# Optimization experiments

Measured on AMD Instinct MI355X. Metric: run time of the kernel, lower is better.

The kernel has to match this reference:

```python
import jax, jax.numpy as jnp
import numpy as np

IN_FEAT = 78
C = 128          # out_channels
H = 8            # nheads (layer 1)
B = 1024         # num graphs / batch
NPG = 32         # nodes per graph
N = B * NPG      # total nodes
EPG = 128        # edges per graph
E = B * EPG
GENE = 18000
PROT = 6688
FP = 2048        # drr/drc fingerprint size
N_TASKS = 1


def _lin(key, fan_in, fan_out):
    kw, kb = jax.random.split(key)
    s = 1.0 / np.sqrt(fan_in)
    W = jax.random.uniform(kw, (fan_in, fan_out), jnp.float32, -s, s)
    b = jax.random.uniform(kb, (fan_out,), jnp.float32, -s, s)
    return W, b


def setup_inputs() -> dict:
    key = jax.random.key(0)
    ks = jax.random.split(key, 32)
    goff = jnp.repeat(jnp.arange(B, dtype=jnp.int64) * NPG, EPG)
    e1s = jax.random.randint(ks[0], (E,), 0, NPG, dtype=jnp.int64) + goff
    e1d = jax.random.randint(ks[1], (E,), 0, NPG, dtype=jnp.int64) + goff
    e2s = jax.random.randint(ks[2], (E,), 0, NPG, dtype=jnp.int64) + goff
    e2d = jax.random.randint(ks[3], (E,), 0, NPG, dtype=jnp.int64) + goff
    inp = {
        "x1": jax.random.normal(ks[4], (N, IN_FEAT), jnp.float32),
        "x2": jax.random.normal(ks[5], (N, IN_FEAT), jnp.float32),
        "gene_exp": jax.random.uniform(ks[6], (B, GENE), jnp.float32),
        "drr": jax.random.uniform(ks[7], (B, FP), jnp.float32),
        "drc": jax.random.uniform(ks[8], (B, FP), jnp.float32),
        "prot_exp": jax.random.normal(ks[9], (B, PROT), jnp.float32),
        "edge_index1": jnp.stack([e1s, e1d]),
        "edge_index2": jnp.stack([e2s, e2d]),
        "batch": jnp.repeat(jnp.arange(B, dtype=jnp.int64), NPG),
    }
    W1, b1 = _lin(ks[10], IN_FEAT, H * C)
    inp.update(W_gat1=W1, b_gat1=b1,
               a_src1=jax.random.normal(ks[11], (H, C), jnp.float32) * 0.1,
               a_dst1=jax.random.normal(ks[12], (H, C), jnp.float32) * 0.1)
    # GAT layer 2: 1024 -> 128, 1 head
    W2, b2 = _lin(ks[13], H * C, C)
    inp.update(W_gat2=W2, b_gat2=b2,
               a_src2=jax.random.normal(ks[14], (1, C), jnp.float32) * 0.1,
               a_dst2=jax.random.normal(ks[15], (1, C), jnp.float32) * 0.1)
    inp["W_fcg"], inp["b_fcg"] = _lin(ks[16], C, C)
    # reduction MLP: gene -> 2048 -> 512 -> 2C
    inp["Wr1"], inp["br1"] = _lin(ks[17], GENE, 2048)
    inp["Wr2"], inp["br2"] = _lin(ks[18], 2048, 512)
    inp["Wr3"], inp["br3"] = _lin(ks[19], 512, 2 * C)
    # prot MLP: 6688 -> 1024 -> 512 -> 2C
    inp["Wp1"], inp["bp1"] = _lin(ks[20], PROT, 1024)
    inp["Wp2"], inp["bp2"] = _lin(ks[21], 1024, 512)
    inp["Wp3"], inp["bp3"] = _lin(ks[22], 512, 2 * C)
    # fingerprint fusion linears
    inp["Wdrr"], inp["bdrr"] = _lin(ks[23], C + FP, C + FP)
    inp["Wdrc"], inp["bdrc"] = _lin(ks[24], C + FP, C + FP)
    # predictor (3 layers): in = 2*(C+FP) + 2C + 2C = 4864 -> 512 -> 256 -> n_tasks
    in_dim = 2 * (C + FP) + 2 * C + 2 * C
    inp["Wf1"], inp["bf1"] = _lin(ks[25], in_dim, 512)
    inp["Wf2"], inp["bf2"] = _lin(ks[26], 512, 256)
    inp["Wout"], inp["bout"] = _lin(ks[27], 256, N_TASKS)
    return inp


def _gat(x, src, dst, W, a_src, a_dst, b, heads, ch):
    n = x.shape[0]
    # add self-loops (PyG GATConv default)
    sl = jnp.arange(n, dtype=src.dtype)
    src = jnp.concatenate([src, sl])
    dst = jnp.concatenate([dst, sl])
    h = (x @ W).reshape(n, heads, ch)                    # [N,H,C]
    a_s = (h * a_src).sum(-1)                            # [N,H]
    a_d = (h * a_dst).sum(-1)
    e = jax.nn.leaky_relu(a_s[src] + a_d[dst], 0.2)      # [E',H]
    m = jax.ops.segment_max(e, dst, num_segments=n)
    ex = jnp.exp(e - m[dst])
    den = jax.ops.segment_sum(ex, dst, num_segments=n)
    alpha = ex / (den[dst] + 1e-16)
    out = jax.ops.segment_sum(h[src] * alpha[:, :, None], dst, num_segments=n)
    return out.reshape(n, heads * ch) + b


def reference(x1, x2, gene_exp, drr, drc, prot_exp,
              W_gat1, b_gat1, a_src1, a_dst1,
              W_gat2, b_gat2, a_src2, a_dst2,
              W_fcg, b_fcg,
              Wr1, br1, Wr2, br2, Wr3, br3,
              Wp1, bp1, Wp2, bp2, Wp3, bp3,
              Wdrr, bdrr, Wdrc, bdrc,
              Wf1, bf1, Wf2, bf2, Wout, bout,
              edge_index1, edge_index2, batch):
    nb = gene_exp.shape[0]

    def drug_branch(x, ei):
        x = jax.nn.elu(_gat(x, ei[0], ei[1], W_gat1, a_src1, a_dst1, b_gat1, H, C))
        x = jax.nn.elu(_gat(x, ei[0], ei[1], W_gat2, a_src2, a_dst2, b_gat2, 1, C))
        x = jax.ops.segment_max(x, batch, num_segments=nb)   # global max pool
        return jax.nn.relu(x @ W_fcg + b_fcg)

    g1 = drug_branch(x1, edge_index1)
    g2 = drug_branch(x2, edge_index2)

    # gene branch: L2 row-normalize then MLP (dropout off at inference)
    norm = jnp.sqrt((gene_exp * gene_exp).sum(1, keepdims=True))
    cell = gene_exp / jnp.maximum(norm, 1e-12)
    cell = jax.nn.relu(cell @ Wr1 + br1)
    cell = jax.nn.relu(cell @ Wr2 + br2)
    cell_vec = jax.nn.relu(cell @ Wr3 + br3)

    # protein branch
    p = prot_exp.reshape(-1, PROT)
    p = jax.nn.elu(p @ Wp1 + bp1)
    p = jax.nn.elu(p @ Wp2 + bp2)
    p = jax.nn.relu(p @ Wp3 + bp3)

    # fingerprint fusion
    d1 = jnp.concatenate([g1, drr], axis=1)
    d2 = jnp.concatenate([g2, drc], axis=1)
    d1 = jax.nn.relu(d1 @ Wdrr + bdrr)
    d2 = jax.nn.relu(d2 @ Wdrc + bdrc)

    y = jnp.concatenate([d1, d2, cell_vec, p], axis=1)
    # 3-layer predictor
    y = jax.nn.relu(y @ Wf1 + bf1)
    y = jax.nn.relu(y @ Wf2 + bf2)
    out = y @ Wout + bout
    return out
```

## Files before the change

kernel.cpp:

```cpp
#include <hip/hip_runtime.h>
#include <math.h>

#define BATCH   1024
#define NPG     32
#define NNODES  (BATCH * NPG)
#define EPG     128
#define INFEAT  78
#define CCH     128
#define NHEAD   8
#define GENE    18000
#define GENEP   18048
#define PROT    6688
#define PROTP   6784
#define FPD     2048

#define ACT_NONE 0
#define ACT_RELU 1
#define ACT_ELU  2

typedef unsigned short ushort_t;
typedef __bf16 bf16x8_t __attribute__((ext_vector_type(8)));
typedef float  f32x4_t  __attribute__((ext_vector_type(4)));

__device__ __forceinline__ float b2f(ushort_t u) {
    return __uint_as_float(((unsigned)u) << 16);
}
__device__ __forceinline__ ushort_t f2b(float f) {
    unsigned x = __float_as_uint(f);
    return (ushort_t)((x + 0x7fffu + ((x >> 16) & 1u)) >> 16);
}

#define GBM 128
#define GBN 128
#define GBK 32

__device__ __forceinline__ void gemm_core(
    const ushort_t* __restrict__ A, const ushort_t* __restrict__ BT,
    int K, int kb, int ke, int row0, int col0,
    ushort_t* Asl, ushort_t* Bsl, f32x4_t acc[4][4])
{
    const int tid  = threadIdx.x;
    const int wave = tid >> 6;
    const int lane = tid & 63;
    const int wr   = wave >> 1;
    const int wc   = wave & 1;
    const int srow = lane >> 2;
    const int skel = (lane & 3) * 8;

    for (int k0 = kb; k0 < ke; k0 += GBK) {
        __syncthreads();
        #pragma unroll
        for (int t = 0; t < 2; ++t) {
            const int rg = wave * 32 + t * 16;
            const ushort_t* ga = A + (size_t)(row0 + rg + srow) * K + k0 + skel;
            __builtin_amdgcn_global_load_lds(
                (const __attribute__((address_space(1))) void*)ga,
                (__attribute__((address_space(3))) void*)&Asl[rg * GBK], 16, 0, 0);
            const ushort_t* gb = BT + (size_t)(col0 + rg + srow) * K + k0 + skel;
            __builtin_amdgcn_global_load_lds(
                (const __attribute__((address_space(1))) void*)gb,
                (__attribute__((address_space(3))) void*)&Bsl[rg * GBK], 16, 0, 0);
        }
        __syncthreads();

        const int fr = lane & 15;
        const int fq = lane >> 4;
        bf16x8_t av[4], bv[4];
        #pragma unroll
        for (int i = 0; i < 4; ++i)
            av[i] = *(const bf16x8_t*)&Asl[(wr * 64 + i * 16 + fr) * GBK + fq * 8];
        #pragma unroll
        for (int j = 0; j < 4; ++j)
            bv[j] = *(const bf16x8_t*)&Bsl[(wc * 64 + j * 16 + fr) * GBK + fq * 8];
        #pragma unroll
        for (int i = 0; i < 4; ++i)
            #pragma unroll
            for (int j = 0; j < 4; ++j)
                acc[i][j] = __builtin_amdgcn_mfma_f32_16x16x32_bf16(
                    av[i], bv[j], acc[i][j], 0, 0, 0);
    }
}

__global__ __launch_bounds__(256) void gemm_bf16_kernel(
    const ushort_t* __restrict__ A, const ushort_t* __restrict__ BT,
    const float* __restrict__ bias, ushort_t* __restrict__ C,
    int M, int N, int K, int act)
{
    __shared__ ushort_t Asl[GBM * GBK];
    __shared__ ushort_t Bsl[GBN * GBK];
    const int lane = threadIdx.x & 63;
    const int wave = threadIdx.x >> 6;
    const int wr = wave >> 1, wc = wave & 1;
    const int row0 = blockIdx.y * GBM;
    const int col0 = blockIdx.x * GBN;

    f32x4_t acc[4][4] = {};
    gemm_core(A, BT, K, 0, K, row0, col0, Asl, Bsl, acc);

    const int fr = lane & 15;
    const int fq = lane >> 4;
    #pragma unroll
    for (int i = 0; i < 4; ++i) {
        #pragma unroll
        for (int j = 0; j < 4; ++j) {
            const int gn = col0 + wc * 64 + j * 16 + fr;
            const float bb = bias ? bias[gn] : 0.0f;
            #pragma unroll
            for (int r = 0; r < 4; ++r) {
                const int gm = row0 + wr * 64 + i * 16 + fq * 4 + r;
                float v = acc[i][j][r] + bb;
                if (act == ACT_RELU)     v = fmaxf(v, 0.0f);
                else if (act == ACT_ELU) v = (v > 0.0f) ? v : (expf(v) - 1.0f);
                C[(size_t)gm * N + gn] = f2b(v);
            }
        }
    }
}

__global__ __launch_bounds__(256) void gemm_bf16_part_kernel(
    const ushort_t* __restrict__ A, const ushort_t* __restrict__ BT,
    float* __restrict__ part, int M, int N, int K, int KC)
{
    __shared__ ushort_t Asl[GBM * GBK];
    __shared__ ushort_t Bsl[GBN * GBK];
    const int lane = threadIdx.x & 63;
    const int wave = threadIdx.x >> 6;
    const int wr = wave >> 1, wc = wave & 1;
    const int row0 = blockIdx.y * GBM;
    const int col0 = blockIdx.x * GBN;
    const int z    = blockIdx.z;
    const int kb   = z * KC;
    const int ke   = min(K, kb + KC);

    f32x4_t acc[4][4] = {};
    gemm_core(A, BT, K, kb, ke, row0, col0, Asl, Bsl, acc);

    const int fr = lane & 15;
    const int fq = lane >> 4;
    float* po = part + (size_t)z * M * N;
    #pragma unroll
    for (int i = 0; i < 4; ++i)
        #pragma unroll
        for (int j = 0; j < 4; ++j) {
            const int gn = col0 + wc * 64 + j * 16 + fr;
            #pragma unroll
            for (int r = 0; r < 4; ++r) {
                const int gm = row0 + wr * 64 + i * 16 + fq * 4 + r;
                po[(size_t)gm * N + gn] = acc[i][j][r];
            }
        }
}

__global__ __launch_bounds__(256) void reduce_kernel(
    const float* __restrict__ part, const float* __restrict__ bias,
    ushort_t* __restrict__ C, int MN, int N, int S, int act)
{
    int i4 = (blockIdx.x * 256 + threadIdx.x) * 4;
    if (i4 >= MN) return;
    float4 s = *(const float4*)&part[i4];
    for (int z = 1; z < S; ++z) {
        float4 v = *(const float4*)&part[(size_t)z * MN + i4];
        s.x += v.x; s.y += v.y; s.z += v.z; s.w += v.w;
    }
    const int n = i4 % N;
    float o[4] = { s.x, s.y, s.z, s.w };
    if (bias) { o[0] += bias[n]; o[1] += bias[n+1]; o[2] += bias[n+2]; o[3] += bias[n+3]; }
    unsigned pk[2];
    ushort_t r[4];
    #pragma unroll
    for (int k = 0; k < 4; ++k) {
        float v = o[k];
        if (act == ACT_RELU)     v = fmaxf(v, 0.0f);
        else if (act == ACT_ELU) v = (v > 0.0f) ? v : (expf(v) - 1.0f);
        r[k] = f2b(v);
    }
    pk[0] = (unsigned)r[0] | ((unsigned)r[1] << 16);
    pk[1] = (unsigned)r[2] | ((unsigned)r[3] << 16);
    *(uint2*)&C[i4] = make_uint2(pk[0], pk[1]);
}

#define DSREAD(dst, addr) asm volatile("ds_read_b128 %0, %1" : "=v"(dst) : "v"(addr))

template <int MH>
__device__ __forceinline__ void read_A8(bf16x8_t (&av)[4][2], unsigned b0, unsigned b1)
{
    DSREAD(av[0][0], b0 + (MH * 4 + 0) * 2048);
    DSREAD(av[0][1], b1 + (MH * 4 + 0) * 2048);
    DSREAD(av[1][0], b0 + (MH * 4 + 1) * 2048);
    DSREAD(av[1][1], b1 + (MH * 4 + 1) * 2048);
    DSREAD(av[2][0], b0 + (MH * 4 + 2) * 2048);
    DSREAD(av[2][1], b1 + (MH * 4 + 2) * 2048);
    DSREAD(av[3][0], b0 + (MH * 4 + 3) * 2048);
    DSREAD(av[3][1], b1 + (MH * 4 + 3) * 2048);
}

template <int NH>
__device__ __forceinline__ void read_B8(bf16x8_t (&bvh)[2][2], unsigned b0, unsigned b1)
{
    DSREAD(bvh[0][0], b0 + (NH * 2 + 0) * 2048);
    DSREAD(bvh[0][1], b1 + (NH * 2 + 0) * 2048);
    DSREAD(bvh[1][0], b0 + (NH * 2 + 1) * 2048);
    DSREAD(bvh[1][1], b1 + (NH * 2 + 1) * 2048);
}

template <int MH, int NH>
__device__ __forceinline__ void mfma_quad(const bf16x8_t (&av)[4][2],
                                          const bf16x8_t (&bvh)[2][2],
                                          f32x4_t (&acc)[8][4])
{
    #pragma unroll
    for (int qq = 0; qq < 4; ++qq)
        #pragma unroll
        for (int pp = 0; pp < 2; ++pp)
            #pragma unroll
            for (int ss = 0; ss < 2; ++ss)
                acc[MH * 4 + qq][NH * 2 + pp] = __builtin_amdgcn_mfma_f32_16x16x32_bf16(
                    av[qq][ss], bvh[pp][ss], acc[MH * 4 + qq][NH * 2 + pp], 0, 0, 0);
}

__device__ __forceinline__ void stage_half8(
    const ushort_t* __restrict__ G, int rc0, int K, int kt,
    unsigned lo0, ushort_t* smemp, int tid)
{
    const int lane = tid & 63;
    const int ce = (((lane & 7) ^ ((lane >> 3) & 7)) << 3);
    #pragma unroll
    for (int j = 0; j < 2; ++j) {
        const int rr = j * 64 + (tid >> 3);
        const ushort_t* g = G + (size_t)(rc0 + rr) * K + kt + ce;
        const unsigned lo = lo0 + (unsigned)((j * 64 + ((tid >> 3) & ~7)) * 128);
        __builtin_amdgcn_global_load_lds(
            (const __attribute__((address_space(1))) void*)g,
            (__attribute__((address_space(3))) void*)((char*)smemp + lo),
            16, 0, 0);
    }
}

#define PH_TAIL(MH, NH, BVH, VM) \
    __builtin_amdgcn_s_barrier(); \
    asm volatile("s_waitcnt lgkmcnt(0)"); \
    __builtin_amdgcn_sched_barrier(0); \
    __builtin_amdgcn_s_setprio(1); \
    mfma_quad<MH, NH>(av, BVH, acc); \
    __builtin_amdgcn_s_setprio(0); \
    __builtin_amdgcn_sched_barrier(0); \
    if (VM) asm volatile("s_waitcnt vmcnt(4)"); \
    __builtin_amdgcn_s_barrier();

__global__ __launch_bounds__(512, 2) void gemm_bf16_8ph_kernel(
    const ushort_t* __restrict__ A, const ushort_t* __restrict__ BT,
    float* __restrict__ part, int M, int N, int K, int IPC)
{
    extern __shared__ ushort_t smem8[];
    const int tid  = threadIdx.x;
    const int lane = tid & 63;
    const int wid  = tid >> 6;
    const int wm = wid >> 2, wn = wid & 3;
    const int fr = lane & 15, fq = lane >> 4;

    const int gx = N >> 8, gy = M >> 8;
    const int nwg = (int)gridDim.x;
    const int q8 = nwg >> 3, r8 = nwg & 7;
    const int xcd = (int)blockIdx.x & 7, sub = (int)blockIdx.x >> 3;
    const int wg = (xcd < r8 ? xcd * (q8 + 1) : r8 * (q8 + 1) + (xcd - r8) * q8) + sub;
    const int bz  = wg / (gx * gy);
    const int rem = wg - bz * gx * gy;
    const int by  = rem / gx;
    const int bx  = rem - by * gx;
    const int row0 = by << 8, col0 = bx << 8;

    const int iters = K >> 7;
    const int k0    = bz * IPC * 128;
    const int nit   = min(IPC, iters - bz * IPC);

    const unsigned SB  = (unsigned)(size_t)(__attribute__((address_space(3))) void*)smem8;
    const unsigned xa  = (unsigned)((fr & 7) << 4);
    const unsigned cs0 = ((unsigned)(fq * 16)) ^ xa;
    const unsigned cs1 = ((unsigned)(64 + fq * 16)) ^ xa;
    const unsigned arow = SB + (unsigned)((wm * 128 + fr) * 128);
    const unsigned brow = SB + 32768u + (unsigned)((wn * 64 + fr) * 128);

    f32x4_t  acc[8][4] = {};
    bf16x8_t av[4][2];
    bf16x8_t bv[2][2][2];

    auto KT = [&](int tt) { int kt = k0 + tt * 64; return kt > K - 64 ? K - 64 : kt; };
    auto STA = [&](int tt, int h) {
        stage_half8(A, row0 + h * 128, K, KT(tt),
                    (unsigned)(((tt & 1) * 65536) + h * 16384), smem8, tid);
    };
    auto STB = [&](int tt, int h) {
        stage_half8(BT, col0 + h * 128, K, KT(tt),
                    (unsigned)(((tt & 1) * 65536) + 32768 + h * 16384), smem8, tid);
    };

    STB(0, 0); STB(0, 1); STA(0, 0); STA(0, 1); STB(1, 0); STB(1, 1);
    asm volatile("s_waitcnt vmcnt(4)");
    __builtin_amdgcn_s_barrier();

    for (int it = 0; it < nit; ++it) {
        const int t = it << 1;
        read_A8<0>(av, arow + cs0, arow + cs1);
        read_B8<0>(bv[0], brow + cs0, brow + cs1);
        STA(t + 1, 0);
        PH_TAIL(0, 0, bv[0], 0)

        read_B8<1>(bv[1], brow + cs0, brow + cs1);
        STA(t + 1, 1);
        PH_TAIL(0, 1, bv[1], 0)

        read_A8<1>(av, arow + cs0, arow + cs1);
        STB(t + 2, 0);
        PH_TAIL(1, 0, bv[0], 0)

        STB(t + 2, 1);
        PH_TAIL(1, 1, bv[1], 1)

        read_A8<0>(av, arow + 65536u + cs0, arow + 65536u + cs1);
        read_B8<0>(bv[0], brow + 65536u + cs0, brow + 65536u + cs1);
        STA(t + 2, 0);
        PH_TAIL(0, 0, bv[0], 0)

        read_B8<1>(bv[1], brow + 65536u + cs0, brow + 65536u + cs1);
        STA(t + 2, 1);
        PH_TAIL(0, 1, bv[1], 0)

        read_A8<1>(av, arow + 65536u + cs0, arow + 65536u + cs1);
        STB(t + 3, 0);
        PH_TAIL(1, 0, bv[0], 0)

        STB(t + 3, 1);
        PH_TAIL(1, 1, bv[1], 1)
    }

    float* po = part + (size_t)bz * M * N;
    const int gmb = row0 + wm * 128 + fq * 4;
    const int gnb = col0 + wn * 64 + fr;
    #pragma unroll
    for (int mi = 0; mi < 8; ++mi)
        #pragma unroll
        for (int nj = 0; nj < 4; ++nj)
            #pragma unroll
            for (int r2 = 0; r2 < 4; ++r2)
                po[(size_t)(gmb + mi * 16 + r2) * N + (gnb + nj * 16)] = acc[mi][nj][r2];
}

__global__ __launch_bounds__(256) void cast_rows_kernel(
    const float* __restrict__ src, const float* __restrict__ rowscale,
    ushort_t* __restrict__ dst, int R, int Cin, int Cpad)
{
    int idx = blockIdx.x * 256 + threadIdx.x;
    if (idx >= R * Cpad) return;
    int r = idx / Cpad, c = idx - r * Cpad;
    float v = 0.0f;
    if (c < Cin) {
        v = src[(size_t)r * Cin + c];
        if (rowscale) v *= rowscale[r];
    }
    dst[idx] = f2b(v);
}

__global__ __launch_bounds__(256) void castT_kernel(
    const float* __restrict__ W, ushort_t* __restrict__ WT,
    int K, int N, int Kpad)
{
    __shared__ float t[32][33];
    const int nb = blockIdx.x * 32, kb = blockIdx.y * 32;
    const int x = threadIdx.x & 31, y = threadIdx.x >> 5;
    #pragma unroll
    for (int yy = 0; yy < 32; yy += 8) {
        int k = kb + y + yy, n = nb + x;
        t[y + yy][x] = (k < K && n < N) ? W[(size_t)k * N + n] : 0.0f;
    }
    __syncthreads();
    #pragma unroll
    for (int yy = 0; yy < 32; yy += 8) {
        int n = nb + y + yy, kk = kb + x;
        if (n < N && kk < Kpad) WT[(size_t)n * Kpad + kk] = f2b(t[x][y + yy]);
    }
}

__device__ __forceinline__ unsigned enc_f(float f) {
    unsigned u = __float_as_uint(f);
    return (u >> 31) ? ~u : (u | 0x80000000u);
}
__device__ __forceinline__ float dec_f(unsigned e) {
    return (e >> 31) ? __uint_as_float(e ^ 0x80000000u) : __uint_as_float(~e);
}

template <int POOL>
__global__ __launch_bounds__(256) void gat_fused_kernel(
    const ushort_t* __restrict__ h, const int* __restrict__ esrc,
    const int* __restrict__ edst, const float* __restrict__ a_src,
    const float* __restrict__ a_dst, const float* __restrict__ bias,
    ushort_t* __restrict__ out, int H)
{
    const int g    = blockIdx.x / H;
    const int hd   = blockIdx.x % H;
    const int tid  = threadIdx.x;
    const int lane = tid & 63;
    const int wave = tid >> 6;
    const int base = g * NPG;
    const int HC   = H * CCH;

    __shared__ float h_l[NPG][CCH];
    __shared__ float At[NPG][NPG];
    __shared__ float asv[CCH], adv[CCH];
    __shared__ float as_l[NPG], ad_l[NPG];
    __shared__ unsigned m_l[NPG];
    __shared__ float den_l[NPG];
    __shared__ float sc_l[EPG + NPG];
    __shared__ unsigned char s_l[EPG + NPG], d_l[EPG + NPG];
    __shared__ float ptmp[2][CCH];

    {
        const int r4 = tid >> 6;
        const int cp = (tid & 63) * 2;
        #pragma unroll
        for (int rr = 0; rr < NPG; rr += 4) {
            const int r = rr + r4;
            unsigned v = *(const unsigned*)(h + (size_t)(base + r) * HC + hd * CCH + cp);
            h_l[r][cp]     = b2f((ushort_t)(v & 0xffff));
            h_l[r][cp + 1] = b2f((ushort_t)(v >> 16));
        }
    }
    #pragma unroll
    for (int i = tid; i < NPG * NPG; i += 256) ((float*)At)[i] = 0.0f;
    if (tid < CCH) asv[tid] = a_src[hd * CCH + tid];
    else           adv[tid - CCH] = a_dst[hd * CCH + tid - CCH];
    if (tid < NPG) { m_l[tid] = 0u; den_l[tid] = 0.0f; }
    __syncthreads();

    for (int n = wave; n < NPG; n += 4) {
        float v0 = h_l[n][lane], v1 = h_l[n][lane + 64];
        float s = v0 * asv[lane] + v1 * asv[lane + 64];
        float d = v0 * adv[lane] + v1 * adv[lane + 64];
        #pragma unroll
        for (int o = 32; o > 0; o >>= 1) {
            s += __shfl_xor(s, o, 64);
            d += __shfl_xor(d, o, 64);
        }
        if (lane == 0) { as_l[n] = s; ad_l[n] = d; }
    }
    __syncthreads();

    if (tid < EPG + NPG) {
        int s, d;
        if (tid < EPG) {
            s = esrc[g * EPG + tid] - base;
            d = edst[g * EPG + tid] - base;
        } else {
            s = d = tid - EPG;
        }
        float e = as_l[s] + ad_l[d];
        e = (e >= 0.0f) ? e : 0.2f * e;
        sc_l[tid] = e;
        s_l[tid] = (unsigned char)s;
        d_l[tid] = (unsigned char)d;
        atomicMax(&m_l[d], enc_f(e));
    }
    __syncthreads();

    if (tid < EPG + NPG) {
        float ex = expf(sc_l[tid] - dec_f(m_l[d_l[tid]]));
        sc_l[tid] = ex;
        atomicAdd(&den_l[d_l[tid]], ex);
    }
    __syncthreads();

    if (tid < EPG + NPG) {
        float al = sc_l[tid] / (den_l[d_l[tid]] + 1e-16f);
        atomicAdd(&At[s_l[tid]][d_l[tid]], al);
    }
    __syncthreads();

    const int c    = tid & 127;
    const int half = tid >> 7;
    float acc[16] = {};
    #pragma unroll 4
    for (int s = 0; s < NPG; ++s) {
        const float hv = h_l[s][c];
        const float4* ap = (const float4*)&At[s][half * 16];
        #pragma unroll
        for (int q = 0; q < 4; ++q) {
            float4 av = ap[q];
            acc[q * 4 + 0] += av.x * hv;
            acc[q * 4 + 1] += av.y * hv;
            acc[q * 4 + 2] += av.z * hv;
            acc[q * 4 + 3] += av.w * hv;
        }
    }

    const float bb = bias[hd * CCH + c];
    if (POOL) {
        float m = -INFINITY;
        #pragma unroll
        for (int r = 0; r < 16; ++r) {
            float v = acc[r] + bb;
            v = (v > 0.0f) ? v : (expf(v) - 1.0f);
            m = fmaxf(m, v);
        }
        ptmp[half][c] = m;
        __syncthreads();
        if (tid < CCH)
            out[(size_t)g * CCH + tid] = f2b(fmaxf(ptmp[0][tid], ptmp[1][tid]));
    } else {
        #pragma unroll
        for (int r = 0; r < 16; ++r) {
            float v = acc[r] + bb;
            v = (v > 0.0f) ? v : (expf(v) - 1.0f);
            out[(size_t)(base + half * 16 + r) * HC + hd * CCH + c] = f2b(v);
        }
    }
}

__global__ __launch_bounds__(256) void rownorm_kernel(
    const float* __restrict__ x, float* __restrict__ inv, int K)
{
    const int row = blockIdx.x;
    const int tid = threadIdx.x;
    const float* xp = x + (size_t)row * K;
    float s = 0.f;
    for (int k = tid; k < K; k += 256) { float v = xp[k]; s += v * v; }
    __shared__ float red[256];
    red[tid] = s;
    __syncthreads();
    for (int o = 128; o > 0; o >>= 1) {
        if (tid < o) red[tid] += red[tid + o];
        __syncthreads();
    }
    if (tid == 0) inv[row] = 1.0f / fmaxf(sqrtf(red[0]), 1e-12f);
}

__global__ __launch_bounds__(256) void copyb_kernel(
    ushort_t* __restrict__ dst, int ld, int off,
    const ushort_t* __restrict__ src, int rows, int cols)
{
    int idx = blockIdx.x * 256 + threadIdx.x;
    if (idx >= rows * cols) return;
    int r = idx / cols, c = idx - r * cols;
    dst[(size_t)r * ld + off + c] = src[idx];
}

__global__ __launch_bounds__(256) void castcols_kernel(
    ushort_t* __restrict__ dst, int ld, int off,
    const float* __restrict__ src, int rows, int cols)
{
    int idx = blockIdx.x * 256 + threadIdx.x;
    if (idx >= rows * cols) return;
    int r = idx / cols, c = idx - r * cols;
    dst[(size_t)r * ld + off + c] = f2b(src[idx]);
}

__global__ __launch_bounds__(256) void final_kernel(
    const ushort_t* __restrict__ y, const float* __restrict__ w,
    const float* __restrict__ b, float* __restrict__ out)
{
    const int row = blockIdx.x;
    const int tid = threadIdx.x;
    float v = b2f(y[(size_t)row * 256 + tid]) * w[tid];
    __shared__ float red[256];
    red[tid] = v;
    __syncthreads();
    for (int o = 128; o > 0; o >>= 1) {
        if (tid < o) red[tid] += red[tid + o];
        __syncthreads();
    }
    if (tid == 0) out[row] = red[0] + b[0];
}

static inline void launch_gemm(const ushort_t* A, const ushort_t* BT,
                               const float* bias, ushort_t* C,
                               int M, int N, int K, int act, hipStream_t stream)
{
    dim3 grid(N / GBN, M / GBM);
    gemm_bf16_kernel<<<grid, 256, 0, stream>>>(A, BT, bias, C, M, N, K, act);
}

static inline void launch_gemm_sk(const ushort_t* A, const ushort_t* BT,
                                  const float* bias, ushort_t* C, float* part,
                                  int M, int N, int K, int S, int act,
                                  hipStream_t stream)
{
    if (S <= 1) { launch_gemm(A, BT, bias, C, M, N, K, act, stream); return; }
    const int iters = K / GBK;
    const int ipc   = (iters + S - 1) / S;
    const int S_eff = (iters + ipc - 1) / ipc;
    const int KC    = ipc * GBK;
    dim3 grid(N / GBN, M / GBM, S_eff);
    gemm_bf16_part_kernel<<<grid, 256, 0, stream>>>(A, BT, part, M, N, K, KC);
    const int MN = M * N;
    reduce_kernel<<<(MN / 4 + 255) / 256, 256, 0, stream>>>(
        part, bias, C, MN, N, S_eff, act);
}

static inline void launch_gemm_8ph(const ushort_t* A, const ushort_t* BT,
                                   const float* bias, ushort_t* C, float* part,
                                   int M, int N, int K, int S, int act,
                                   hipStream_t stream)
{
    const int iters = K >> 7;
    const int ipc   = (iters + S - 1) / S;
    const int S_eff = (iters + ipc - 1) / ipc;
    const int gx = N >> 8, gy = M >> 8;
    const int nwg = gx * gy * S_eff;
    static bool attr_done = false;
    if (!attr_done) {
        (void)hipFuncSetAttribute((const void*)gemm_bf16_8ph_kernel,
                                  hipFuncAttributeMaxDynamicSharedMemorySize, 131072);
        attr_done = true;
    }
    gemm_bf16_8ph_kernel<<<dim3(nwg), 512, 131072, stream>>>(A, BT, part, M, N, K, ipc);
    const int MN = M * N;
    reduce_kernel<<<(MN / 4 + 255) / 256, 256, 0, stream>>>(
        part, bias, C, MN, N, S_eff, act);
}

static inline void launch_castT(const float* W, ushort_t* WT, int K, int N,
                                int Kpad, hipStream_t stream)
{
    dim3 grid((N + 31) / 32, (Kpad + 31) / 32);
    castT_kernel<<<grid, 256, 0, stream>>>(W, WT, K, N, Kpad);
}

extern "C" void kernel_launch(void* const* d_in, const int* in_sizes, int n_in,
                              void* d_out, int out_size, void* d_ws, size_t ws_size,
                              hipStream_t stream)
{
    const float* x1      = (const float*)d_in[0];
    const float* x2      = (const float*)d_in[1];
    const float* gene    = (const float*)d_in[2];
    const float* drr     = (const float*)d_in[3];
    const float* drc     = (const float*)d_in[4];
    const float* prot    = (const float*)d_in[5];
    const int*   ei1     = (const int*)d_in[6];
    const int*   ei2     = (const int*)d_in[7];
    const float* W_gat1  = (const float*)d_in[9];
    const float* b_gat1  = (const float*)d_in[10];
    const float* a_src1  = (const float*)d_in[11];
    const float* a_dst1  = (const float*)d_in[12];
    const float* W_gat2  = (const float*)d_in[13];
    const float* b_gat2  = (const float*)d_in[14];
    const float* a_src2  = (const float*)d_in[15];
    const float* a_dst2  = (const float*)d_in[16];
    const float* W_fcg   = (const float*)d_in[17];
    const float* b_fcg   = (const float*)d_in[18];
    const float* Wr1     = (const float*)d_in[19];
    const float* br1     = (const float*)d_in[20];
    const float* Wr2     = (const float*)d_in[21];
    const float* br2     = (const float*)d_in[22];
    const float* Wr3     = (const float*)d_in[23];
    const float* br3     = (const float*)d_in[24];
    const float* Wp1     = (const float*)d_in[25];
    const float* bp1     = (const float*)d_in[26];
    const float* Wp2     = (const float*)d_in[27];
    const float* bp2     = (const float*)d_in[28];
    const float* Wp3     = (const float*)d_in[29];
    const float* bp3     = (const float*)d_in[30];
    const float* Wdrr    = (const float*)d_in[31];
    const float* bdrr    = (const float*)d_in[32];
    const float* Wdrc    = (const float*)d_in[33];
    const float* bdrc    = (const float*)d_in[34];
    const float* Wf1     = (const float*)d_in[35];
    const float* bf1     = (const float*)d_in[36];
    const float* Wf2     = (const float*)d_in[37];
    const float* bf2     = (const float*)d_in[38];
    const float* Wout    = (const float*)d_in[39];
    const float* bout    = (const float*)d_in[40];
    float* outp = (float*)d_out;

    char* ws = (char*)d_ws;
    size_t off = 0;
    auto alloc = [&](size_t bytes) -> char* {
        char* r = ws + off;
        off += (bytes + 255) & ~(size_t)255;
        return r;
    };

    char* BIG0 = alloc(134217728);
    char* BIG1 = alloc(67108864);

    ushort_t* go1f   = (ushort_t*)BIG0;
    ushort_t* h1     = (ushort_t*)BIG1;
    float*    part   = (float*)BIG1;
    ushort_t* WT_r1  = (ushort_t*)(BIG0 + 0);
    ushort_t* gene_nb= (ushort_t*)(BIG0 + 73924608);
    ushort_t* cell1  = (ushort_t*)(BIG0 + 110886912);
    ushort_t* WT_r2  = (ushort_t*)(BIG0 + 115081216);
    ushort_t* WT_p2  = (ushort_t*)(BIG0 + 117178368);
    ushort_t* WT_p1  = (ushort_t*)(BIG0 + 118226944);

    ushort_t* xb     = (ushort_t*)alloc((size_t)NNODES * 96 * 2);
    char*     h2reg  = alloc((size_t)2 * NNODES * 128 * 2);
    char*     catreg = alloc((size_t)2 * 1024 * 2176 * 2);
    ushort_t* h2f    = (ushort_t*)h2reg;
    ushort_t* protb  = (ushort_t*)h2reg;
    ushort_t* cat1   = (ushort_t*)catreg;
    ushort_t* cat2   = (ushort_t*)(catreg + (size_t)1024 * 2176 * 2);
    ushort_t* pooled = (ushort_t*)alloc((size_t)2 * BATCH * 128 * 2);
    ushort_t* gpair  = (ushort_t*)alloc((size_t)2 * BATCH * 128 * 2);
    float*    invn   = (float*)alloc((size_t)BATCH * 4);
    ushort_t* cvec   = (ushort_t*)alloc((size_t)BATCH * 256 * 2);
    ushort_t* pvec   = (ushort_t*)alloc((size_t)BATCH * 256 * 2);
    ushort_t* y1     = (ushort_t*)alloc((size_t)BATCH * 512 * 2);
    ushort_t* y2     = (ushort_t*)alloc((size_t)BATCH * 256 * 2);
    ushort_t* WT_g1  = (ushort_t*)alloc((size_t)1024 * 96 * 2);
    ushort_t* WT_g2  = (ushort_t*)alloc((size_t)128 * 1024 * 2);
    ushort_t* WT_fcg = (ushort_t*)alloc((size_t)128 * 128 * 2);
    ushort_t* WT_r3  = (ushort_t*)alloc((size_t)256 * 512 * 2);
    ushort_t* WT_p3  = (ushort_t*)alloc((size_t)256 * 512 * 2);
    ushort_t* WT_f2  = (ushort_t*)alloc((size_t)256 * 512 * 2);
    ushort_t* WT_drr = (ushort_t*)alloc((size_t)2176 * 2176 * 2);
    ushort_t* WT_drc = (ushort_t*)alloc((size_t)2176 * 2176 * 2);
    ushort_t* WT_f1  = (ushort_t*)alloc((size_t)512 * 4864 * 2);
    ushort_t* p1b    = (ushort_t*)alloc((size_t)1024 * 1024 * 2);
    ushort_t* p2b    = (ushort_t*)alloc((size_t)1024 * 512 * 2);
    ushort_t* cell2  = (ushort_t*)alloc((size_t)1024 * 512 * 2);
    ushort_t* d1     = (ushort_t*)alloc((size_t)1024 * 2176 * 2);
    ushort_t* d2     = (ushort_t*)alloc((size_t)1024 * 2176 * 2);
    ushort_t* ybuf   = (ushort_t*)alloc((size_t)1024 * 4864 * 2);

    const int E = in_sizes[6] / 2;

    launch_castT(W_gat1, WT_g1, INFEAT, 1024, 96, stream);
    launch_castT(W_gat2, WT_g2, 1024, 128, 1024, stream);
    launch_castT(W_fcg,  WT_fcg, 128, 128, 128, stream);

    for (int drug = 0; drug < 2; drug++) {
        const float* x  = drug ? x2 : x1;
        const int*   es = (drug ? ei2 : ei1);
        const int*   ed = es + E;
        ushort_t* go1d = go1f + (size_t)drug * NNODES * 1024;

        cast_rows_kernel<<<(NNODES * 96 + 255) / 256, 256, 0, stream>>>(
            x, nullptr, xb, NNODES, INFEAT, 96);
        launch_gemm(xb, WT_g1, nullptr, h1, NNODES, 1024, 96, ACT_NONE, stream);
        gat_fused_kernel<0><<<BATCH * NHEAD, 256, 0, stream>>>(
            h1, es, ed, a_src1, a_dst1, b_gat1, go1d, NHEAD);
    }

    launch_gemm(go1f, WT_g2, nullptr, h2f, 2 * NNODES, 128, 1024, ACT_NONE, stream);

    launch_castT(Wr1, WT_r1, GENE, 2048, GENEP, stream);
    launch_castT(Wr2, WT_r2, 2048, 512, 2048, stream);
    launch_castT(Wp1, WT_p1, PROT, 1024, PROTP, stream);
    launch_castT(Wp2, WT_p2, 1024, 512, 1024, stream);
    launch_castT(Wr3, WT_r3, 512, 256, 512, stream);
    launch_castT(Wp3, WT_p3, 512, 256, 512, stream);
    launch_castT(Wf2, WT_f2, 512, 256, 512, stream);
    launch_castT(Wdrr, WT_drr, 2176, 2176, 2176, stream);
    launch_castT(Wdrc, WT_drc, 2176, 2176, 2176, stream);
    launch_castT(Wf1, WT_f1, 4864, 512, 4864, stream);

    for (int drug = 0; drug < 2; drug++) {
        const int* es = (drug ? ei2 : ei1);
        const int* ed = es + E;
        gat_fused_kernel<1><<<BATCH, 256, 0, stream>>>(
            h2f + (size_t)drug * NNODES * 128, es, ed,
            a_src2, a_dst2, b_gat2, pooled + (size_t)drug * BATCH * 128, 1);
    }
    launch_gemm(pooled, WT_fcg, b_fcg, gpair, 2 * BATCH, 128, 128, ACT_RELU, stream);

    rownorm_kernel<<<BATCH, 256, 0, stream>>>(gene, invn, GENE);
    cast_rows_kernel<<<(BATCH * GENEP + 255) / 256, 256, 0, stream>>>(
        gene, invn, gene_nb, BATCH, GENE, GENEP);
    launch_gemm_8ph(gene_nb, WT_r1, br1, cell1, part, BATCH, 2048, GENEP, 8, ACT_RELU, stream);
    launch_gemm_sk(cell1, WT_r2, br2, cell2, part, BATCH, 512, 2048, 8, ACT_RELU, stream);
    launch_gemm_sk(cell2, WT_r3, br3, cvec, part, BATCH, 256, 512, 4, ACT_RELU, stream);

    cast_rows_kernel<<<(BATCH * PROTP + 255) / 256, 256, 0, stream>>>(
        prot, nullptr, protb, BATCH, PROT, PROTP);
    launch_gemm_8ph(protb, WT_p1, bp1, p1b, part, BATCH, 1024, PROTP, 16, ACT_ELU, stream);
    launch_gemm_sk(p1b, WT_p2, bp2, p2b, part, BATCH, 512, 1024, 4, ACT_ELU, stream);
    launch_gemm_sk(p2b, WT_p3, bp3, pvec, part, BATCH, 256, 512, 4, ACT_RELU, stream);

    {
        int n = BATCH * CCH;
        copyb_kernel<<<(n + 255) / 256, 256, 0, stream>>>(cat1, 2176, 0, gpair, BATCH, CCH);
        copyb_kernel<<<(n + 255) / 256, 256, 0, stream>>>(cat2, 2176, 0, gpair + BATCH * CCH, BATCH, CCH);
        n = BATCH * FPD;
        castcols_kernel<<<(n + 255) / 256, 256, 0, stream>>>(cat1, 2176, CCH, drr, BATCH, FPD);
        castcols_kernel<<<(n + 255) / 256, 256, 0, stream>>>(cat2, 2176, CCH, drc, BATCH, FPD);
    }
    launch_gemm_sk(cat1, WT_drr, bdrr, d1, part, BATCH, 2176, 2176, 4, ACT_RELU, stream);
    launch_gemm_sk(cat2, WT_drc, bdrc, d2, part, BATCH, 2176, 2176, 4, ACT_RELU, stream);

    {
        int n = BATCH * 2176;
        copyb_kernel<<<(n + 255) / 256, 256, 0, stream>>>(ybuf, 4864, 0,    d1, BATCH, 2176);
        copyb_kernel<<<(n + 255) / 256, 256, 0, stream>>>(ybuf, 4864, 2176, d2, BATCH, 2176);
        n = BATCH * 256;
        copyb_kernel<<<(n + 255) / 256, 256, 0, stream>>>(ybuf, 4864, 4352, cvec, BATCH, 256);
        copyb_kernel<<<(n + 255) / 256, 256, 0, stream>>>(ybuf, 4864, 4608, pvec, BATCH, 256);
    }
    launch_gemm_sk(ybuf, WT_f1, bf1, y1, part, BATCH, 512, 4864, 8, ACT_RELU, stream);
    launch_gemm_sk(y1, WT_f2, bf2, y2, part, BATCH, 256, 512, 4, ACT_RELU, stream);
    final_kernel<<<BATCH, 256, 0, stream>>>(y2, Wout, bout, outp);
}
```

Baseline: 1.188 ms.

## Compute GAT aggregation with bf16 MFMA using split-precision attention matrix

Replaces the scalar FP32 attention-times-features aggregation in the fused GAT kernel with MFMA 16x16x32 bf16 instructions. The attention matrix is split into high and low bf16 parts to keep near-fp32 accuracy. Node features stay in LDS as bf16 and are transposed into a swizzled layout. LDS use drops because the feature and attention tiles share one buffer, and the edge-index loads are hoisted to the kernel start to overlap latency. In exchange it adds a transpose step, extra syncs and a small precision change on the feature operand.

```diff
diff --git a/kernel.cpp b/kernel.cpp
--- a/kernel.cpp
+++ b/kernel.cpp
@@ -388,6 +388,10 @@
     return (e >> 31) ? __uint_as_float(e ^ 0x80000000u) : __uint_as_float(~e);
 }
 
+__device__ __forceinline__ unsigned swz32(int row, int chunk) {
+    return (unsigned)((row << 6) + ((chunk ^ (row & 3)) << 4));
+}
+
 template <int POOL>
 __global__ __launch_bounds__(256) void gat_fused_kernel(
     const ushort_t* __restrict__ h, const int* __restrict__ esrc,
@@ -403,7 +407,8 @@
     const int base = g * NPG;
     const int HC   = H * CCH;
 
-    __shared__ float h_l[NPG][CCH];
+    __shared__ __align__(16) char uni[NPG * CCH * 2];
+    __shared__ __align__(16) ushort_t hT[CCH * 32];
     __shared__ float At[NPG][NPG];
     __shared__ float asv[CCH], adv[CCH];
     __shared__ float as_l[NPG], ad_l[NPG];
@@ -411,7 +416,18 @@
     __shared__ float den_l[NPG];
     __shared__ float sc_l[EPG + NPG];
     __shared__ unsigned char s_l[EPG + NPG], d_l[EPG + NPG];
-    __shared__ float ptmp[2][CCH];
+
+    ushort_t (*h_row)[CCH] = (ushort_t(*)[CCH])uni;
+    ushort_t* AtH = (ushort_t*)uni;
+    ushort_t* AtL = (ushort_t*)(uni + 2048);
+
+    int es_r = 0, ed_r = 0;
+    if (tid < EPG) {
+        es_r = esrc[g * EPG + tid] - base;
+        ed_r = edst[g * EPG + tid] - base;
+    } else if (tid < EPG + NPG) {
+        es_r = ed_r = tid - EPG;
+    }
 
     {
         const int r4 = tid >> 6;
@@ -420,8 +436,7 @@
         for (int rr = 0; rr < NPG; rr += 4) {
             const int r = rr + r4;
             unsigned v = *(const unsigned*)(h + (size_t)(base + r) * HC + hd * CCH + cp);
-            h_l[r][cp]     = b2f((ushort_t)(v & 0xffff));
-            h_l[r][cp + 1] = b2f((ushort_t)(v >> 16));
+            *(unsigned*)&h_row[r][cp] = v;
         }
     }
     #pragma unroll
@@ -432,7 +447,7 @@
     __syncthreads();
 
     for (int n = wave; n < NPG; n += 4) {
-        float v0 = h_l[n][lane], v1 = h_l[n][lane + 64];
+        float v0 = b2f(h_row[n][lane]), v1 = b2f(h_row[n][lane + 64]);
         float s = v0 * asv[lane] + v1 * asv[lane + 64];
         float d = v0 * adv[lane] + v1 * adv[lane + 64];
         #pragma unroll
@@ -442,22 +457,31 @@
         }
         if (lane == 0) { as_l[n] = s; ad_l[n] = d; }
     }
+    {
+        const int c  = tid & 127;
+        const int s0 = (tid >> 7) * 16;
+        #pragma unroll
+        for (int hh = 0; hh < 2; ++hh) {
+            const int sb = s0 + hh * 8;
+            unsigned pk[4];
+            #pragma unroll
+            for (int p = 0; p < 4; ++p) {
+                unsigned lo = h_row[sb + 2 * p][c];
+                unsigned hi = h_row[sb + 2 * p + 1][c];
+                pk[p] = lo | (hi << 16);
+            }
+            *(uint4*)((char*)hT + swz32(c, sb >> 3)) = make_uint4(pk[0], pk[1], pk[2], pk[3]);
+        }
+    }
     __syncthreads();
 
     if (tid < EPG + NPG) {
-        int s, d;
-        if (tid < EPG) {
-            s = esrc[g * EPG + tid] - base;
-            d = edst[g * EPG + tid] - base;
-        } else {
-            s = d = tid - EPG;
-        }
-        float e = as_l[s] + ad_l[d];
+        float e = as_l[es_r] + ad_l[ed_r];
         e = (e >= 0.0f) ? e : 0.2f * e;
         sc_l[tid] = e;
-        s_l[tid] = (unsigned char)s;
-        d_l[tid] = (unsigned char)d;
-        atomicMax(&m_l[d], enc_f(e));
+        s_l[tid] = (unsigned char)es_r;
+        d_l[tid] = (unsigned char)ed_r;
+        atomicMax(&m_l[ed_r], enc_f(e));
     }
     __syncthreads();
 
@@ -474,42 +498,72 @@
     }
     __syncthreads();
 
-    const int c    = tid & 127;
-    const int half = tid >> 7;
-    float acc[16] = {};
-    #pragma unroll 4
-    for (int s = 0; s < NPG; ++s) {
-        const float hv = h_l[s][c];
-        const float4* ap = (const float4*)&At[s][half * 16];
+    {
+        const int d  = tid >> 3;
+        const int s4 = (tid & 7) * 4;
+        float v0 = At[s4 + 0][d], v1 = At[s4 + 1][d];
+        float v2 = At[s4 + 2][d], v3 = At[s4 + 3][d];
+        ushort_t h0 = f2b(v0), h1 = f2b(v1), h2 = f2b(v2), h3 = f2b(v3);
+        ushort_t l0 = f2b(v0 - b2f(h0)), l1 = f2b(v1 - b2f(h1));
+        ushort_t l2 = f2b(v2 - b2f(h2)), l3 = f2b(v3 - b2f(h3));
+        const unsigned a = swz32(d, s4 >> 3) + (unsigned)((s4 & 7) * 2);
+        *(uint2*)((char*)AtH + a) = make_uint2((unsigned)h0 | ((unsigned)h1 << 16),
+                                               (unsigned)h2 | ((unsigned)h3 << 16));
+        *(uint2*)((char*)AtL + a) = make_uint2((unsigned)l0 | ((unsigned)l1 << 16),
+                                               (unsigned)l2 | ((unsigned)l3 << 16));
+    }
+    __syncthreads();
+
+    const int fr = lane & 15, fq = lane >> 4;
+    const int dblk  = wave & 1;
+    const int cbase = (wave >> 1) * 64;
+
+    bf16x8_t aH = *(const bf16x8_t*)((char*)AtH + swz32(dblk * 16 + fr, fq));
+    bf16x8_t aL = *(const bf16x8_t*)((char*)AtL + swz32(dblk * 16 + fr, fq));
+    bf16x8_t bfr[4];
+    #pragma unroll
+    for (int q = 0; q < 4; ++q)
+        bfr[q] = *(const bf16x8_t*)((char*)hT + swz32(cbase + q * 16 + fr, fq));
+
+    f32x4_t acc[4] = {};
+    #pragma unroll
+    for (int q = 0; q < 4; ++q) {
+        acc[q] = __builtin_amdgcn_mfma_f32_16x16x32_bf16(aH, bfr[q], acc[q], 0, 0, 0);
+        acc[q] = __builtin_amdgcn_mfma_f32_16x16x32_bf16(aL, bfr[q], acc[q], 0, 0, 0);
+    }
+
+    if (POOL) {
+        float* pool2 = (float*)At;
         #pragma unroll
         for (int q = 0; q < 4; ++q) {
-            float4 av = ap[q];
-            acc[q * 4 + 0] += av.x * hv;
-            acc[q * 4 + 1] += av.y * hv;
-            acc[q * 4 + 2] += av.z * hv;
-            acc[q * 4 + 3] += av.w * hv;
+            const int c = cbase + q * 16 + fr;
+            const float bb = bias[hd * CCH + c];
+            float m = -INFINITY;
+            #pragma unroll
+            for (int r = 0; r < 4; ++r) {
+                float v = acc[q][r] + bb;
+                v = (v > 0.0f) ? v : (expf(v) - 1.0f);
+                m = fmaxf(m, v);
+            }
+            m = fmaxf(m, __shfl_xor(m, 16, 64));
+            m = fmaxf(m, __shfl_xor(m, 32, 64));
+            if (fq == 0) pool2[dblk * CCH + c] = m;
         }
-    }
-
-    const float bb = bias[hd * CCH + c];
-    if (POOL) {
-        float m = -INFINITY;
-        #pragma unroll
-        for (int r = 0; r < 16; ++r) {
-            float v = acc[r] + bb;
-            v = (v > 0.0f) ? v : (expf(v) - 1.0f);
-            m = fmaxf(m, v);
-        }
-        ptmp[half][c] = m;
         __syncthreads();
         if (tid < CCH)
-            out[(size_t)g * CCH + tid] = f2b(fmaxf(ptmp[0][tid], ptmp[1][tid]));
+            out[(size_t)g * CCH + tid] = f2b(fmaxf(pool2[tid], pool2[CCH + tid]));
     } else {
         #pragma unroll
-        for (int r = 0; r < 16; ++r) {
-            float v = acc[r] + bb;
-            v = (v > 0.0f) ? v : (expf(v) - 1.0f);
-            out[(size_t)(base + half * 16 + r) * HC + hd * CCH + c] = f2b(v);
+        for (int q = 0; q < 4; ++q) {
+            const int c = cbase + q * 16 + fr;
+            const float bb = bias[hd * CCH + c];
+            #pragma unroll
+            for (int r = 0; r < 4; ++r) {
+                const int d = dblk * 16 + fq * 4 + r;
+                float v = acc[q][r] + bb;
+                v = (v > 0.0f) ? v : (expf(v) - 1.0f);
+                out[(size_t)(base + d) * HC + hd * CCH + c] = f2b(v);
+            }
         }
     }
 }
```

New measurement: 1.134 ms. 4.5% less time.
